# Performance work log

Hardware: AMD Instinct MI355X
Metric: run time of the kernel (lower is better)

## Reference

```python
import jax, jax.numpy as jnp
import numpy as np

N, T, D, H = 256, 128, 512, 1024


def setup_inputs() -> dict:
    key = jax.random.key(0)
    k_x, k_A, k_Wx, k_Wh, k_Wa = jax.random.split(key, 5)
    x = jax.random.normal(k_x, (N, T, D), dtype=jnp.float32)
    A = jax.random.normal(k_A, (N, H, 4, 4), dtype=jnp.float32)
    Wx = jax.random.normal(k_Wx, (D, 4 * H), dtype=jnp.float32) / np.sqrt(D)
    Wh = jax.random.normal(k_Wh, (H, 4 * H), dtype=jnp.float32) / np.sqrt(H)
    Wattn = jax.random.normal(k_Wa, (H, 4 * H), dtype=jnp.float32) / np.sqrt(H)
    b = jnp.zeros((4 * H,), dtype=jnp.float32)
    return {"x": x, "A": A, "Wx": Wx, "Wh": Wh, "Wattn": Wattn, "b": b}


def _attention_lstm(x, A, Wx, Wh, Wattn, b):
    # A: (N, H, 4, 4) -> flatten spatial to (N, H, 16)
    A_flat = A.reshape(A.shape[0], A.shape[1], -1)
    h0 = A_flat.mean(axis=2)  # (N, H)
    c0 = h0
    Hdim = h0.shape[1]
    scale = 1.0 / jnp.sqrt(jnp.asarray(Hdim, dtype=x.dtype))

    def step(carry, x_t):
        prev_h, prev_c = carry
        # scaled dot-product attention over 16 spatial locations
        scores = jnp.einsum("nh,nhs->ns", prev_h, A_flat) * scale  # (N, 16)
        w = jax.nn.softmax(scores, axis=1)
        attn = jnp.einsum("nhs,ns->nh", A_flat, w)  # (N, H)
        # fused LSTM gates
        a = x_t @ Wx + prev_h @ Wh + attn @ Wattn + b  # (N, 4H)
        i = jax.nn.sigmoid(a[:, 0:Hdim])
        f = jax.nn.sigmoid(a[:, Hdim:2 * Hdim])
        o = jax.nn.sigmoid(a[:, 2 * Hdim:3 * Hdim])
        g = jnp.tanh(a[:, 3 * Hdim:4 * Hdim])
        next_c = f * prev_c + i * g
        next_h = o * jnp.tanh(next_c)
        return (next_h, next_c), next_h

    x_tnd = jnp.swapaxes(x, 0, 1)  # (T, N, D)
    _, h_tnh = jax.lax.scan(step, (h0, c0), x_tnd)
    return jnp.swapaxes(h_tnh, 0, 1)  # (N, T, H)


def reference(x, A, Wx, Wh, Wattn, b):
    return _attention_lstm(x, A, Wx, Wh, Wattn, b)
```

## Files before the change

kernel.cpp:

```cpp
#include <hip/hip_runtime.h>
#include <math.h>

#define NB 256
#define TT 128
#define DD 512
#define HH 1024
#define KHX 1536
#define KFB 2560
#define BK 128

typedef _Float16 half_t;
typedef _Float16 half8 __attribute__((ext_vector_type(8)));
typedef _Float16 half4v __attribute__((ext_vector_type(4)));
typedef float f32x4 __attribute__((ext_vector_type(4)));


__global__ __launch_bounds__(256) void k_trans(const float* __restrict__ src,
        half_t* __restrict__ dst, int kstride, int koff, int nkt) {
    __shared__ half_t tile[64][65];
    int bk = blockIdx.x % nkt;
    int bn = blockIdx.x / nkt;
    int k0 = bk * 64, n0 = bn * 64;
    #pragma unroll
    for (int i = 0; i < 16; ++i) {
        int idx = i * 256 + threadIdx.x;
        int r = idx >> 6, c = idx & 63;
        tile[c][r] = (half_t)src[(size_t)(k0 + r) * 4096 + n0 + c];
    }
    __syncthreads();
    #pragma unroll
    for (int i = 0; i < 16; ++i) {
        int idx = i * 256 + threadIdx.x;
        int r = idx >> 6, c = idx & 63;
        dst[(size_t)(n0 + r) * kstride + koff + k0 + c] = tile[r][c];
    }
}

__global__ __launch_bounds__(256) void k_convA(const float* __restrict__ A,
        half_t* __restrict__ A16, half_t* __restrict__ AsT,
        float* __restrict__ cbuf, half_t* __restrict__ h16,
        float* __restrict__ sc0, float* __restrict__ sc1, float* __restrict__ sc2) {
    __shared__ float sred[4][16];
    int n = blockIdx.x, tid = threadIdx.x;
    float ps[16];
    #pragma unroll
    for (int s = 0; s < 16; ++s) ps[s] = 0.f;
    #pragma unroll
    for (int r = 0; r < 4; ++r) {
        int h = tid + r * 256;
        const float4* ap = (const float4*)(A + ((size_t)n * HH + h) * 16);
        float4 v0 = ap[0], v1 = ap[1], v2 = ap[2], v3 = ap[3];
        float a[16];
        a[0]=v0.x; a[1]=v0.y; a[2] =v0.z; a[3] =v0.w;
        a[4]=v1.x; a[5]=v1.y; a[6] =v1.z; a[7] =v1.w;
        a[8]=v2.x; a[9]=v2.y; a[10]=v2.z; a[11]=v2.w;
        a[12]=v3.x; a[13]=v3.y; a[14]=v3.z; a[15]=v3.w;
        float hv = 0.f;
        #pragma unroll
        for (int s = 0; s < 16; ++s) hv += a[s];
        hv *= (1.f / 16.f);
        size_t ci = (size_t)n * HH + h;
        cbuf[ci] = hv;
        h16[ci] = (half_t)hv;
        half8 q0, q1;
        #pragma unroll
        for (int s = 0; s < 8; ++s) { q0[s] = (half_t)a[s]; q1[s] = (half_t)a[s + 8]; }
        *(half8*)(A16 + ci * 16) = q0;
        *(half8*)(A16 + ci * 16 + 8) = q1;
        #pragma unroll
        for (int s = 0; s < 16; ++s)
            AsT[(size_t)n * 16 * HH + (size_t)s * HH + h] = (half_t)a[s];
        #pragma unroll
        for (int s = 0; s < 16; ++s) ps[s] += hv * a[s];
    }
    #pragma unroll
    for (int off = 32; off; off >>= 1)
        #pragma unroll
        for (int s = 0; s < 16; ++s) ps[s] += __shfl_xor(ps[s], off, 64);
    int wave = tid >> 6;
    if ((tid & 63) == 0)
        #pragma unroll
        for (int s = 0; s < 16; ++s) sred[wave][s] = ps[s];
    __syncthreads();
    if (tid < 16) {
        sc0[n * 16 + tid] = sred[0][tid] + sred[1][tid] + sred[2][tid] + sred[3][tid];
        sc1[n * 16 + tid] = 0.f;
        sc2[n * 16 + tid] = 0.f;
    }
}

__global__ __launch_bounds__(256) void k_gemm_G(const half_t* __restrict__ AsT,
        const half_t* __restrict__ WaT, half_t* __restrict__ G16) {
    __shared__ half_t sAs[16][BK + 8];
    __shared__ half_t sB[4][16][BK + 8];
    int bid = blockIdx.x;
    int n = bid >> 6, jt = bid & 63;
    int j0 = jt * 16;
    int tid = threadIdx.x, wv = tid >> 6, lane = tid & 63;
    f32x4 acc = {};
    int srB = tid >> 2, scB = (tid & 3) * 32;
    int gB = srB >> 4, jcB = srB & 15;
    for (int it = 0; it < HH / BK; ++it) {
        int k0 = it * BK;
        if (tid < 128) {
            int r = tid >> 3, c = (tid & 7) * 16;
            const uint4* sp = (const uint4*)(AsT + (size_t)n * 16 * HH + (size_t)r * HH + k0 + c);
            uint4 u0 = sp[0], u1 = sp[1];
            *(uint4*)&sAs[r][c] = u0;
            *(uint4*)&sAs[r][c + 8] = u1;
        }
        {
            const half_t* src = WaT + ((size_t)(gB * HH + j0 + jcB)) * HH + k0 + scB;
            uint4 u0 = ((const uint4*)src)[0];
            uint4 u1 = ((const uint4*)src)[1];
            uint4 u2 = ((const uint4*)src)[2];
            uint4 u3 = ((const uint4*)src)[3];
            *((uint4*)&sB[gB][jcB][scB])      = u0;
            *((uint4*)&sB[gB][jcB][scB + 8])  = u1;
            *((uint4*)&sB[gB][jcB][scB + 16]) = u2;
            *((uint4*)&sB[gB][jcB][scB + 24]) = u3;
        }
        __syncthreads();
        int row16 = lane & 15, kg = lane >> 4;
        #pragma unroll
        for (int kc = 0; kc < BK / 32; ++kc) {
            half8 bf = *(const half8*)&sB[wv][row16][kc * 32 + kg * 8];
            half8 af = *(const half8*)&sAs[row16][kc * 32 + kg * 8];
            acc = __builtin_amdgcn_mfma_f32_16x16x32_f16(af, bf, acc, 0, 0, 0);
        }
        __syncthreads();
    }
    int col = lane & 15, rbase = (lane >> 4) * 4;
    size_t jf = (size_t)wv * HH + j0 + col;
    half4v o;
    o[0] = (half_t)acc[0]; o[1] = (half_t)acc[1];
    o[2] = (half_t)acc[2]; o[3] = (half_t)acc[3];
    *(half4v*)(G16 + ((size_t)n * 4096 + jf) * 16 + rbase) = o;
}

union LdsS {
    struct {
        half_t sA[32][BK + 8];
        half_t sB[4][16][BK + 8];
    } s;
    float pe[4][32][16];
};

__global__ __launch_bounds__(256) void k_step(const float* __restrict__ x,
        const half_t* __restrict__ h16c, half_t* __restrict__ h16n,
        const half_t* __restrict__ WhxT, const half_t* __restrict__ A16,
        const half_t* __restrict__ G16, const float* __restrict__ b,
        float* __restrict__ cbuf, const float* __restrict__ scC,
        float* __restrict__ scN, float* __restrict__ scZ,
        float* __restrict__ out, int t) {
    __shared__ LdsS L;
    __shared__ float wlds[32][16];
    int bid = blockIdx.x;
    int xcd = bid & 7, slot = bid >> 3;
    int mtile = slot & 7, jtile = slot >> 3;
    int n0 = mtile * 32;
    int j0 = xcd * 128 + jtile * 16;
    int tid = threadIdx.x, wv = tid >> 6, lane = tid & 63;

    if (bid < 16) scZ[bid * 256 + tid] = 0.f;
    if (tid < 32) {
        int n = n0 + tid;
        const float4* sp = (const float4*)(scC + n * 16);
        float4 u0 = sp[0], u1 = sp[1], u2 = sp[2], u3 = sp[3];
        float sc[16] = {u0.x, u0.y, u0.z, u0.w, u1.x, u1.y, u1.z, u1.w,
                        u2.x, u2.y, u2.z, u2.w, u3.x, u3.y, u3.z, u3.w};
        float m = -1e30f;
        #pragma unroll
        for (int s = 0; s < 16; ++s) { sc[s] *= 0.03125f; m = fmaxf(m, sc[s]); }
        float den = 0.f;
        #pragma unroll
        for (int s = 0; s < 16; ++s) { sc[s] = expf(sc[s] - m); den += sc[s]; }
        float inv = 1.f / den;
        #pragma unroll
        for (int s = 0; s < 16; ++s) wlds[tid][s] = sc[s] * inv;
    }

    f32x4 acc[2] = {};
    int srA = tid >> 3, scA = (tid & 7) * 16;
    int srB = tid >> 2, scB = (tid & 3) * 32;
    int gB = srB >> 4, jcB = srB & 15;

    for (int it = 0; it < KHX / BK; ++it) {
        int k0 = it * BK;
        {
            int n = n0 + srA;
            if (k0 < DD) {
                const float* src = x + ((size_t)n * TT + t) * DD + k0 + scA;
                float4 v0 = ((const float4*)src)[0];
                float4 v1 = ((const float4*)src)[1];
                float4 v2 = ((const float4*)src)[2];
                float4 v3 = ((const float4*)src)[3];
                half8 p0, p1;
                p0[0] = (half_t)v0.x; p0[1] = (half_t)v0.y; p0[2] = (half_t)v0.z; p0[3] = (half_t)v0.w;
                p0[4] = (half_t)v1.x; p0[5] = (half_t)v1.y; p0[6] = (half_t)v1.z; p0[7] = (half_t)v1.w;
                p1[0] = (half_t)v2.x; p1[1] = (half_t)v2.y; p1[2] = (half_t)v2.z; p1[3] = (half_t)v2.w;
                p1[4] = (half_t)v3.x; p1[5] = (half_t)v3.y; p1[6] = (half_t)v3.z; p1[7] = (half_t)v3.w;
                *(half8*)&L.s.sA[srA][scA]     = p0;
                *(half8*)&L.s.sA[srA][scA + 8] = p1;
            } else {
                const half_t* srch = h16c + (size_t)n * HH + (k0 - DD) + scA;
                uint4 u0 = ((const uint4*)srch)[0];
                uint4 u1 = ((const uint4*)srch)[1];
                *((uint4*)&L.s.sA[srA][scA])     = u0;
                *((uint4*)&L.s.sA[srA][scA + 8]) = u1;
            }
        }
        {
            const half_t* src = WhxT + ((size_t)(gB * HH + j0 + jcB)) * KHX + k0 + scB;
            uint4 u0 = ((const uint4*)src)[0];
            uint4 u1 = ((const uint4*)src)[1];
            uint4 u2 = ((const uint4*)src)[2];
            uint4 u3 = ((const uint4*)src)[3];
            *((uint4*)&L.s.sB[gB][jcB][scB])      = u0;
            *((uint4*)&L.s.sB[gB][jcB][scB + 8])  = u1;
            *((uint4*)&L.s.sB[gB][jcB][scB + 16]) = u2;
            *((uint4*)&L.s.sB[gB][jcB][scB + 24]) = u3;
        }
        __syncthreads();
        int row16 = lane & 15, kg = lane >> 4;
        #pragma unroll
        for (int kc = 0; kc < BK / 32; ++kc) {
            half8 bf = *(const half8*)&L.s.sB[wv][row16][kc * 32 + kg * 8];
            #pragma unroll
            for (int m = 0; m < 2; ++m) {
                half8 af = *(const half8*)&L.s.sA[row16 + m * 16][kc * 32 + kg * 8];
                acc[m] = __builtin_amdgcn_mfma_f32_16x16x32_f16(af, bf, acc[m], 0, 0, 0);
            }
        }
        __syncthreads();
    }
    {
        int col = lane & 15, rbase = (lane >> 4) * 4;
        #pragma unroll
        for (int m = 0; m < 2; ++m)
            #pragma unroll
            for (int q = 0; q < 4; ++q)
                L.pe[wv][m * 16 + rbase + q][col] = acc[m][q];
    }
    __syncthreads();
    #pragma unroll
    for (int q2 = 0; q2 < 2; ++q2) {
        int idx = tid + q2 * 256;
        int r = idx >> 4, jc = idx & 15;
        int n = n0 + r, j = j0 + jc;
        float wv16[16];
        #pragma unroll
        for (int s = 0; s < 16; ++s) wv16[s] = wlds[r][s];
        float v[4];
        v[0] = L.pe[0][r][jc] + b[j];
        v[1] = L.pe[1][r][jc] + b[HH + j];
        v[2] = L.pe[2][r][jc] + b[2 * HH + j];
        v[3] = L.pe[3][r][jc] + b[3 * HH + j];
        #pragma unroll
        for (int g = 0; g < 4; ++g) {
            const half8* gq = (const half8*)(G16 + ((size_t)n * 4096 + g * HH + j) * 16);
            half8 ga = gq[0], gb2 = gq[1];
            float a0 = 0.f;
            #pragma unroll
            for (int s = 0; s < 8; ++s)
                a0 += wv16[s] * (float)ga[s] + wv16[s + 8] * (float)gb2[s];
            v[g] += a0;
        }
        float ig = 1.f / (1.f + expf(-v[0]));
        float fg = 1.f / (1.f + expf(-v[1]));
        float og = 1.f / (1.f + expf(-v[2]));
        float gg = tanhf(v[3]);
        size_t ci = (size_t)n * HH + j;
        float cp = cbuf[ci];
        float cn = fg * cp + ig * gg;
        cbuf[ci] = cn;
        float hv = og * tanhf(cn);
        out[((size_t)n * TT + t) * HH + j] = hv;
        h16n[ci] = (half_t)hv;
        const half8* ap = (const half8*)(A16 + ci * 16);
        half8 a0 = ap[0], a1 = ap[1];
        float p[16];
        #pragma unroll
        for (int s = 0; s < 8; ++s) { p[s] = hv * (float)a0[s]; p[s + 8] = hv * (float)a1[s]; }
        #pragma unroll
        for (int msk = 1; msk < 16; msk <<= 1)
            #pragma unroll
            for (int s = 0; s < 16; ++s) p[s] += __shfl_xor(p[s], msk, 64);
        float myp = 0.f;
        #pragma unroll
        for (int s = 0; s < 16; ++s) myp = (jc == s) ? p[s] : myp;
        atomicAdd(scN + n * 16 + jc, myp);
    }
}


__global__ __launch_bounds__(256) void fb_wconv(const float* __restrict__ Wx,
        const float* __restrict__ Wh, const float* __restrict__ Wa,
        half_t* __restrict__ WT) {
    __shared__ half_t tile[64][65];
    int bk = blockIdx.x % 40;
    int bn = blockIdx.x / 40;
    int k0 = bk * 64, n0 = bn * 64;
    #pragma unroll
    for (int i = 0; i < 16; ++i) {
        int idx = i * 256 + threadIdx.x;
        int r = idx >> 6, c = idx & 63;
        int k = k0 + r, n = n0 + c;
        float v;
        if (k < DD)            v = Wx[(size_t)k * 4096 + n];
        else if (k < DD + HH)  v = Wh[(size_t)(k - DD) * 4096 + n];
        else                   v = Wa[(size_t)(k - DD - HH) * 4096 + n];
        tile[c][r] = (half_t)v;
    }
    __syncthreads();
    #pragma unroll
    for (int i = 0; i < 16; ++i) {
        int idx = i * 256 + threadIdx.x;
        int r = idx >> 6, c = idx & 63;
        WT[(size_t)(n0 + r) * KFB + k0 + c] = tile[r][c];
    }
}

__global__ __launch_bounds__(256) void fb_init(const float* __restrict__ A,
        float* __restrict__ h0, float* __restrict__ c0) {
    int n = blockIdx.x;
    #pragma unroll
    for (int r = 0; r < 4; ++r) {
        int h = threadIdx.x + r * 256;
        const float4* ap = (const float4*)(A + ((size_t)n * HH + h) * 16);
        float s = 0.f;
        #pragma unroll
        for (int q = 0; q < 4; ++q) {
            float4 v = ap[q];
            s += v.x + v.y + v.z + v.w;
        }
        s *= (1.f / 16.f);
        h0[n * HH + h] = s;
        c0[n * HH + h] = s;
    }
}

__global__ __launch_bounds__(256) void fb_attn(const float* __restrict__ A,
        const float* __restrict__ hprev, long long hstride,
        half_t* __restrict__ h16, half_t* __restrict__ attn16) {
    __shared__ float sh[HH];
    __shared__ float sred[4][16];
    int n = blockIdx.x;
    const float* hp = hprev + (size_t)n * hstride;
    #pragma unroll
    for (int r = 0; r < 4; ++r) {
        int h = threadIdx.x + r * 256;
        float v = hp[h];
        sh[h] = v;
        h16[n * HH + h] = (half_t)v;
    }
    __syncthreads();
    float a[4][16];
    float ps[16];
    #pragma unroll
    for (int s = 0; s < 16; ++s) ps[s] = 0.f;
    #pragma unroll
    for (int r = 0; r < 4; ++r) {
        int h = threadIdx.x + r * 256;
        const float4* ap = (const float4*)(A + ((size_t)n * HH + h) * 16);
        float4 v0 = ap[0], v1 = ap[1], v2 = ap[2], v3 = ap[3];
        a[r][0] = v0.x;  a[r][1] = v0.y;  a[r][2]  = v0.z;  a[r][3]  = v0.w;
        a[r][4] = v1.x;  a[r][5] = v1.y;  a[r][6]  = v1.z;  a[r][7]  = v1.w;
        a[r][8] = v2.x;  a[r][9] = v2.y;  a[r][10] = v2.z;  a[r][11] = v2.w;
        a[r][12] = v3.x; a[r][13] = v3.y; a[r][14] = v3.z;  a[r][15] = v3.w;
        float hh = sh[h];
        #pragma unroll
        for (int s = 0; s < 16; ++s) ps[s] += hh * a[r][s];
    }
    #pragma unroll
    for (int off = 32; off; off >>= 1)
        #pragma unroll
        for (int s = 0; s < 16; ++s) ps[s] += __shfl_xor(ps[s], off, 64);
    int wave = threadIdx.x >> 6;
    if ((threadIdx.x & 63) == 0)
        #pragma unroll
        for (int s = 0; s < 16; ++s) sred[wave][s] = ps[s];
    __syncthreads();
    float sc[16], m = -1e30f;
    #pragma unroll
    for (int s = 0; s < 16; ++s) {
        sc[s] = (sred[0][s] + sred[1][s] + sred[2][s] + sred[3][s]) * 0.03125f;
        m = fmaxf(m, sc[s]);
    }
    float den = 0.f;
    #pragma unroll
    for (int s = 0; s < 16; ++s) { sc[s] = expf(sc[s] - m); den += sc[s]; }
    float inv = 1.f / den;
    #pragma unroll
    for (int r = 0; r < 4; ++r) {
        int h = threadIdx.x + r * 256;
        float acc = 0.f;
        #pragma unroll
        for (int s = 0; s < 16; ++s) acc += a[r][s] * sc[s];
        attn16[n * HH + h] = (half_t)(acc * inv);
    }
}

union LdsFB {
    struct {
        half_t sA[32][BK + 8];
        half_t sB[4][16][BK + 8];
    } s;
    float pe[4][32][16];
};

__global__ __launch_bounds__(256) void fb_gemm(const float* __restrict__ x,
        const half_t* __restrict__ h16, const half_t* __restrict__ attn16,
        const half_t* __restrict__ WT, const float* __restrict__ b,
        float* __restrict__ cbuf, float* __restrict__ out, int t) {
    __shared__ LdsFB L;
    int bid = blockIdx.x;
    int xcd = bid & 7;
    int slot = bid >> 3;
    int mtile = slot & 7;
    int jtile = slot >> 3;
    int m0 = mtile * 32;
    int j0 = xcd * 128 + jtile * 16;
    int tid = threadIdx.x;
    int wv = tid >> 6, lane = tid & 63;
    f32x4 acc[2] = {};
    int srA = tid >> 3, scA = (tid & 7) * 16;
    int srB = tid >> 2, scB = (tid & 3) * 32;
    int gB = srB >> 4, jcB = srB & 15;
    for (int it = 0; it < KFB / BK; ++it) {
        int k0 = it * BK;
        {
            int n = m0 + srA;
            if (k0 < DD) {
                const float* src = x + ((size_t)n * TT + t) * DD + k0 + scA;
                float4 v0 = ((const float4*)src)[0];
                float4 v1 = ((const float4*)src)[1];
                float4 v2 = ((const float4*)src)[2];
                float4 v3 = ((const float4*)src)[3];
                half8 p0, p1;
                p0[0] = (half_t)v0.x; p0[1] = (half_t)v0.y; p0[2] = (half_t)v0.z; p0[3] = (half_t)v0.w;
                p0[4] = (half_t)v1.x; p0[5] = (half_t)v1.y; p0[6] = (half_t)v1.z; p0[7] = (half_t)v1.w;
                p1[0] = (half_t)v2.x; p1[1] = (half_t)v2.y; p1[2] = (half_t)v2.z; p1[3] = (half_t)v2.w;
                p1[4] = (half_t)v3.x; p1[5] = (half_t)v3.y; p1[6] = (half_t)v3.z; p1[7] = (half_t)v3.w;
                *(half8*)&L.s.sA[srA][scA]     = p0;
                *(half8*)&L.s.sA[srA][scA + 8] = p1;
            } else {
                const half_t* srch = (k0 < DD + HH)
                    ? (h16    + (size_t)n * HH + (k0 - DD)      + scA)
                    : (attn16 + (size_t)n * HH + (k0 - DD - HH) + scA);
                uint4 u0 = ((const uint4*)srch)[0];
                uint4 u1 = ((const uint4*)srch)[1];
                *((uint4*)&L.s.sA[srA][scA])     = u0;
                *((uint4*)&L.s.sA[srA][scA + 8]) = u1;
            }
        }
        {
            const half_t* src = WT + ((size_t)(gB * HH + j0 + jcB)) * KFB + k0 + scB;
            uint4 u0 = ((const uint4*)src)[0];
            uint4 u1 = ((const uint4*)src)[1];
            uint4 u2 = ((const uint4*)src)[2];
            uint4 u3 = ((const uint4*)src)[3];
            *((uint4*)&L.s.sB[gB][jcB][scB])      = u0;
            *((uint4*)&L.s.sB[gB][jcB][scB + 8])  = u1;
            *((uint4*)&L.s.sB[gB][jcB][scB + 16]) = u2;
            *((uint4*)&L.s.sB[gB][jcB][scB + 24]) = u3;
        }
        __syncthreads();
        int row16 = lane & 15, kg = lane >> 4;
        #pragma unroll
        for (int kc = 0; kc < BK / 32; ++kc) {
            half8 bf = *(const half8*)&L.s.sB[wv][row16][kc * 32 + kg * 8];
            #pragma unroll
            for (int m = 0; m < 2; ++m) {
                half8 af = *(const half8*)&L.s.sA[row16 + m * 16][kc * 32 + kg * 8];
                acc[m] = __builtin_amdgcn_mfma_f32_16x16x32_f16(af, bf, acc[m], 0, 0, 0);
            }
        }
        __syncthreads();
    }
    {
        int col = lane & 15, rbase = (lane >> 4) * 4;
        #pragma unroll
        for (int m = 0; m < 2; ++m)
            #pragma unroll
            for (int q = 0; q < 4; ++q)
                L.pe[wv][m * 16 + rbase + q][col] = acc[m][q];
    }
    __syncthreads();
    #pragma unroll
    for (int q2 = 0; q2 < 2; ++q2) {
        int idx = tid + q2 * 256;
        int r = idx >> 4, jc = idx & 15;
        int n = m0 + r, j = j0 + jc;
        float vi = L.pe[0][r][jc] + b[j];
        float vf = L.pe[1][r][jc] + b[HH + j];
        float vo = L.pe[2][r][jc] + b[2 * HH + j];
        float vg = L.pe[3][r][jc] + b[3 * HH + j];
        float ig = 1.f / (1.f + expf(-vi));
        float fg = 1.f / (1.f + expf(-vf));
        float og = 1.f / (1.f + expf(-vo));
        float gg = tanhf(vg);
        size_t ci = (size_t)n * HH + j;
        float cp = cbuf[ci];
        float cn = fg * cp + ig * gg;
        cbuf[ci] = cn;
        out[((size_t)n * TT + t) * HH + j] = og * tanhf(cn);
    }
}


extern "C" void kernel_launch(void* const* d_in, const int* in_sizes, int n_in,
                              void* d_out, int out_size, void* d_ws, size_t ws_size,
                              hipStream_t stream) {
    const float* x  = (const float*)d_in[0];
    const float* A  = (const float*)d_in[1];
    const float* Wx = (const float*)d_in[2];
    const float* Wh = (const float*)d_in[3];
    const float* Wa = (const float*)d_in[4];
    const float* b  = (const float*)d_in[5];
    float* out = (float*)d_out;
    char* ws = (char*)d_ws;

    if (ws_size >= 73449472ULL) {
        half_t* WhxT = (half_t*)(ws);
        half_t* WaT  = (half_t*)(ws + 12582912);
        half_t* A16  = (half_t*)(ws + 20971520);
        half_t* AsT  = (half_t*)(ws + 29360128);
        half_t* G16  = (half_t*)(ws + 37748736);
        half_t* h16a = (half_t*)(ws + 71303168);
        half_t* h16b = (half_t*)(ws + 71827456);
        float*  cb   = (float*) (ws + 72351744);
        float*  sc0  = (float*) (ws + 73400320);
        float*  sc1  = (float*) (ws + 73416704);
        float*  sc2  = (float*) (ws + 73433088);
        float* scb[3] = {sc0, sc1, sc2};

        hipLaunchKernelGGL(k_trans, dim3(8 * 64),  dim3(256), 0, stream, Wx, WhxT, KHX, 0,   8);
        hipLaunchKernelGGL(k_trans, dim3(16 * 64), dim3(256), 0, stream, Wh, WhxT, KHX, 512, 16);
        hipLaunchKernelGGL(k_trans, dim3(16 * 64), dim3(256), 0, stream, Wa, WaT,  HH,  0,   16);
        hipLaunchKernelGGL(k_convA, dim3(256), dim3(256), 0, stream,
                           A, A16, AsT, cb, h16a, sc0, sc1, sc2);
        hipLaunchKernelGGL(k_gemm_G, dim3(NB * 64), dim3(256), 0, stream, AsT, WaT, G16);
        for (int t = 0; t < TT; ++t) {
            float* scC = scb[t % 3];
            float* scN = scb[(t + 1) % 3];
            float* scZ = scb[(t + 2) % 3];
            half_t* h16c = (t & 1) ? h16b : h16a;
            half_t* h16n = (t & 1) ? h16a : h16b;
            hipLaunchKernelGGL(k_step, dim3(512), dim3(256), 0, stream,
                               x, h16c, h16n, WhxT, A16, G16, b, cb, scC, scN, scZ, out, t);
        }
    } else {
        half_t* WT  = (half_t*)ws;
        float*  h0  = (float*)(ws + 20971520);
        float*  cb  = (float*)(ws + 22020096);
        half_t* h16 = (half_t*)(ws + 23068672);
        half_t* a16 = (half_t*)(ws + 23592960);
        hipLaunchKernelGGL(fb_wconv, dim3(2560), dim3(256), 0, stream, Wx, Wh, Wa, WT);
        hipLaunchKernelGGL(fb_init, dim3(256), dim3(256), 0, stream, A, h0, cb);
        for (int t = 0; t < TT; ++t) {
            const float* hp = (t == 0) ? h0 : (out + (size_t)(t - 1) * HH);
            long long hstride = (t == 0) ? (long long)HH : (long long)TT * HH;
            hipLaunchKernelGGL(fb_attn, dim3(256), dim3(256), 0, stream, A, hp, hstride, h16, a16);
            hipLaunchKernelGGL(fb_gemm, dim3(512), dim3(256), 0, stream,
                               x, h16, a16, WT, b, cb, out, t);
        }
    }
}
```

Measured before the change: 4.641 ms.

## Replace per-timestep kernel launches with persistent kernel using grid barrier

Adds a persistent k_steps kernel that loops over all 128 timesteps inside one launch of 512 blocks, synchronising with an atomic counter/flag grid barrier instead of launching a kernel per step. x is pre-converted to fp16, c state is kept in registers, and the gate GEMM uses a larger K tile with register prefetch. This removes per-step launch overhead and reloading of cell state, but depends on all 512 blocks being co-resident (checked via occupancy query) and adds barrier spin cost each step.

After: 4.646 ms. Within noise of the previous version (+0.1%).

```diff
diff --git a/kernel.cpp b/kernel.cpp
--- a/kernel.cpp
+++ b/kernel.cpp
@@ -8,6 +8,9 @@
 #define KHX 1536
 #define KFB 2560
 #define BK 128
+#define BKP 256
+#define NIT (KHX / BKP)
+#define NBLK 512
 
 typedef _Float16 half_t;
 typedef _Float16 half8 __attribute__((ext_vector_type(8)));
@@ -33,6 +36,20 @@
         int idx = i * 256 + threadIdx.x;
         int r = idx >> 6, c = idx & 63;
         dst[(size_t)(n0 + r) * kstride + koff + k0 + c] = tile[r][c];
+    }
+}
+
+__global__ __launch_bounds__(256) void k_convX(const float* __restrict__ x,
+        half_t* __restrict__ x16) {
+    size_t base = ((size_t)blockIdx.x * 256 + threadIdx.x) * 32;
+    #pragma unroll
+    for (int u = 0; u < 4; ++u) {
+        float4 a = ((const float4*)(x + base))[2 * u];
+        float4 c = ((const float4*)(x + base))[2 * u + 1];
+        half8 p;
+        p[0] = (half_t)a.x; p[1] = (half_t)a.y; p[2] = (half_t)a.z; p[3] = (half_t)a.w;
+        p[4] = (half_t)c.x; p[5] = (half_t)c.y; p[6] = (half_t)c.z; p[7] = (half_t)c.w;
+        ((half8*)(x16 + base))[u] = p;
     }
 }
 
@@ -137,6 +154,207 @@
     o[2] = (half_t)acc[2]; o[3] = (half_t)acc[3];
     *(half4v*)(G16 + ((size_t)n * 4096 + jf) * 16 + rbase) = o;
 }
+
+
+union LdsP {
+    struct {
+        half_t sA[32][BKP + 8];
+        half_t sB[64][BKP + 8];
+    } s;
+    float pe[4][32][16];
+};
+
+__device__ __forceinline__ void grid_sync(int* cnt, int* flag, int inst) {
+    __syncthreads();
+    if (threadIdx.x == 0) {
+        __threadfence();
+        int prev = __hip_atomic_fetch_add(cnt, 1, __ATOMIC_ACQ_REL,
+                                          __HIP_MEMORY_SCOPE_AGENT);
+        if (prev == NBLK * (inst + 1) - 1) {
+            __hip_atomic_store(flag, inst + 1, __ATOMIC_RELEASE,
+                               __HIP_MEMORY_SCOPE_AGENT);
+        } else {
+            int guard = 0;
+            while (__hip_atomic_load(flag, __ATOMIC_RELAXED,
+                                     __HIP_MEMORY_SCOPE_AGENT) < inst + 1) {
+                __builtin_amdgcn_s_sleep(2);
+                if (++guard > (1 << 24)) break;
+            }
+        }
+        __threadfence();
+    }
+    __syncthreads();
+}
+
+__global__ __launch_bounds__(256, 2) void k_steps(
+        const half_t* __restrict__ x16, const half_t* __restrict__ WhxT,
+        const half_t* __restrict__ A16, const half_t* __restrict__ G16,
+        const float* __restrict__ b, const float* __restrict__ cbuf,
+        float* __restrict__ sc0, float* __restrict__ sc1, float* __restrict__ sc2,
+        half_t* __restrict__ h16a, half_t* __restrict__ h16b,
+        float* __restrict__ out, int* __restrict__ bar) {
+    __shared__ LdsP L;
+    __shared__ float wlds[32][16];
+    int bid = blockIdx.x;
+    int xcd = bid & 7, slot = bid >> 3;
+    int mtile = slot & 7, jtile = slot >> 3;
+    int n0 = mtile * 32;
+    int j0 = xcd * 128 + jtile * 16;
+    int tid = threadIdx.x, wv = tid >> 6, lane = tid & 63;
+    int srA = tid >> 3, scA = (tid & 7) * 32;
+    int srB = tid >> 2, scB = (tid & 3) * 64;
+    int gB = srB >> 4, jcB = srB & 15;
+    int row16 = lane & 15, kg = lane >> 4;
+
+    float* scbuf[3] = {sc0, sc1, sc2};
+    int* cnt = bar;
+    int* flag = bar + 32;
+
+    float bb[2][4];
+    half8 ha[2][2];
+    float creg[2];
+    const half8* gp[2][4];
+    #pragma unroll
+    for (int q2 = 0; q2 < 2; ++q2) {
+        int idx = tid + q2 * 256;
+        int r = idx >> 4, jc = idx & 15;
+        int n = n0 + r, j = j0 + jc;
+        bb[q2][0] = b[j];          bb[q2][1] = b[HH + j];
+        bb[q2][2] = b[2 * HH + j]; bb[q2][3] = b[3 * HH + j];
+        size_t ci = (size_t)n * HH + j;
+        const half8* ap = (const half8*)(A16 + ci * 16);
+        ha[q2][0] = ap[0]; ha[q2][1] = ap[1];
+        creg[q2] = cbuf[ci];
+        #pragma unroll
+        for (int g = 0; g < 4; ++g)
+            gp[q2][g] = (const half8*)(G16 + ((size_t)n * 4096 + g * HH + j) * 16);
+    }
+    half_t* h16c = h16a;
+    half_t* h16n = h16b;
+
+    for (int t = 0; t < TT; ++t) {
+        float* scC = scbuf[t % 3];
+        float* scN = scbuf[(t + 1) % 3];
+        float* scZ = scbuf[(t + 2) % 3];
+        if (bid < 16) scZ[bid * 256 + tid] = 0.f;
+        if (tid < 32) {
+            int n = n0 + tid;
+            const float4* sp = (const float4*)(scC + n * 16);
+            float4 u0 = sp[0], u1 = sp[1], u2 = sp[2], u3 = sp[3];
+            float sc[16] = {u0.x, u0.y, u0.z, u0.w, u1.x, u1.y, u1.z, u1.w,
+                            u2.x, u2.y, u2.z, u2.w, u3.x, u3.y, u3.z, u3.w};
+            float m = -1e30f;
+            #pragma unroll
+            for (int s = 0; s < 16; ++s) { sc[s] *= 0.03125f; m = fmaxf(m, sc[s]); }
+            float den = 0.f;
+            #pragma unroll
+            for (int s = 0; s < 16; ++s) { sc[s] = expf(sc[s] - m); den += sc[s]; }
+            float inv = 1.f / den;
+            #pragma unroll
+            for (int s = 0; s < 16; ++s) wlds[tid][s] = sc[s] * inv;
+        }
+
+        f32x4 acc[2] = {};
+        uint4 rA[4], rB[8];
+        {
+            const half_t* sa = x16 + ((size_t)(n0 + srA) * TT + t) * DD + scA;
+            #pragma unroll
+            for (int u = 0; u < 4; ++u) rA[u] = ((const uint4*)sa)[u];
+            const half_t* sb = WhxT + (size_t)(gB * HH + j0 + jcB) * KHX + scB;
+            #pragma unroll
+            for (int u = 0; u < 8; ++u) rB[u] = ((const uint4*)sb)[u];
+        }
+        for (int it = 0; it < NIT; ++it) {
+            __syncthreads();
+            #pragma unroll
+            for (int u = 0; u < 4; ++u) *((uint4*)&L.s.sA[srA][scA + u * 8]) = rA[u];
+            #pragma unroll
+            for (int u = 0; u < 8; ++u)
+                *((uint4*)&L.s.sB[gB * 16 + jcB][scB + u * 8]) = rB[u];
+            __syncthreads();
+            if (it + 1 < NIT) {
+                int k0 = (it + 1) * BKP;
+                const half_t* sa = (k0 < DD)
+                    ? x16 + ((size_t)(n0 + srA) * TT + t) * DD + k0 + scA
+                    : h16c + (size_t)(n0 + srA) * HH + (k0 - DD) + scA;
+                #pragma unroll
+                for (int u = 0; u < 4; ++u) rA[u] = ((const uint4*)sa)[u];
+                const half_t* sb = WhxT + (size_t)(gB * HH + j0 + jcB) * KHX + k0 + scB;
+                #pragma unroll
+                for (int u = 0; u < 8; ++u) rB[u] = ((const uint4*)sb)[u];
+            }
+            #pragma unroll
+            for (int kc = 0; kc < BKP / 32; ++kc) {
+                half8 bf = *(const half8*)&L.s.sB[wv * 16 + row16][kc * 32 + kg * 8];
+                #pragma unroll
+                for (int m = 0; m < 2; ++m) {
+                    half8 af = *(const half8*)&L.s.sA[row16 + m * 16][kc * 32 + kg * 8];
+                    acc[m] = __builtin_amdgcn_mfma_f32_16x16x32_f16(af, bf, acc[m], 0, 0, 0);
+                }
+            }
+        }
+        __syncthreads();
+        {
+            int col = lane & 15, rbase = (lane >> 4) * 4;
+            #pragma unroll
+            for (int m = 0; m < 2; ++m)
+                #pragma unroll
+                for (int q = 0; q < 4; ++q)
+                    L.pe[wv][m * 16 + rbase + q][col] = acc[m][q];
+        }
+        __syncthreads();
+        #pragma unroll
+        for (int q2 = 0; q2 < 2; ++q2) {
+            int idx = tid + q2 * 256;
+            int r = idx >> 4, jc = idx & 15;
+            int n = n0 + r, j = j0 + jc;
+            float wv16[16];
+            #pragma unroll
+            for (int s = 0; s < 16; ++s) wv16[s] = wlds[r][s];
+            float v[4];
+            v[0] = L.pe[0][r][jc] + bb[q2][0];
+            v[1] = L.pe[1][r][jc] + bb[q2][1];
+            v[2] = L.pe[2][r][jc] + bb[q2][2];
+            v[3] = L.pe[3][r][jc] + bb[q2][3];
+            #pragma unroll
+            for (int g = 0; g < 4; ++g) {
+                half8 ga = gp[q2][g][0], gb2 = gp[q2][g][1];
+                float a0 = 0.f;
+                #pragma unroll
+                for (int s = 0; s < 8; ++s)
+                    a0 += wv16[s] * (float)ga[s] + wv16[s + 8] * (float)gb2[s];
+                v[g] += a0;
+            }
+            float ig = 1.f / (1.f + expf(-v[0]));
+            float fg = 1.f / (1.f + expf(-v[1]));
+            float og = 1.f / (1.f + expf(-v[2]));
+            float gg = tanhf(v[3]);
+            float cn = fg * creg[q2] + ig * gg;
+            creg[q2] = cn;
+            float hv = og * tanhf(cn);
+            out[((size_t)n * TT + t) * HH + j] = hv;
+            h16n[(size_t)n * HH + j] = (half_t)hv;
+            half8 a0 = ha[q2][0], a1 = ha[q2][1];
+            float p[16];
+            #pragma unroll
+            for (int s = 0; s < 8; ++s) {
+                p[s] = hv * (float)a0[s];
+                p[s + 8] = hv * (float)a1[s];
+            }
+            #pragma unroll
+            for (int msk = 1; msk < 16; msk <<= 1)
+                #pragma unroll
+                for (int s = 0; s < 16; ++s) p[s] += __shfl_xor(p[s], msk, 64);
+            float myp = 0.f;
+            #pragma unroll
+            for (int s = 0; s < 16; ++s) myp = (jc == s) ? p[s] : myp;
+            atomicAdd(scN + n * 16 + jc, myp);
+        }
+        if (t + 1 < TT) grid_sync(cnt, flag, t);
+        half_t* tmp = h16c; h16c = h16n; h16n = tmp;
+    }
+}
+
 
 union LdsS {
     struct {
@@ -521,7 +739,37 @@
     float* out = (float*)d_out;
     char* ws = (char*)d_ws;
 
-    if (ws_size >= 73449472ULL) {
+    int maxb = 0;
+    hipError_t oe = hipOccupancyMaxActiveBlocksPerMultiprocessor(&maxb, k_steps, 256, 0);
+    bool persistent_ok = (oe == hipSuccess && maxb >= 2);
+
+    if (ws_size >= 107004160ULL && persistent_ok) {
+        half_t* WhxT = (half_t*)(ws);
+        half_t* WaT  = (half_t*)(ws + 12582912);
+        half_t* A16  = (half_t*)(ws + 20971520);
+        half_t* AsT  = (half_t*)(ws + 29360128);
+        half_t* G16  = (half_t*)(ws + 37748736);
+        half_t* h16a = (half_t*)(ws + 71303168);
+        half_t* h16b = (half_t*)(ws + 71827456);
+        float*  cb   = (float*) (ws + 72351744);
+        float*  sc0  = (float*) (ws + 73400320);
+        float*  sc1  = (float*) (ws + 73416704);
+        float*  sc2  = (float*) (ws + 73433088);
+        half_t* x16  = (half_t*)(ws + 73449472);
+        int*    bar  = (int*)   (ws + 107003904);
+
+        hipLaunchKernelGGL(k_trans, dim3(8 * 64),  dim3(256), 0, stream, Wx, WhxT, KHX, 0,   8);
+        hipLaunchKernelGGL(k_trans, dim3(16 * 64), dim3(256), 0, stream, Wh, WhxT, KHX, 512, 16);
+        hipLaunchKernelGGL(k_trans, dim3(16 * 64), dim3(256), 0, stream, Wa, WaT,  HH,  0,   16);
+        hipLaunchKernelGGL(k_convX, dim3(2048), dim3(256), 0, stream, x, x16);
+        hipLaunchKernelGGL(k_convA, dim3(256), dim3(256), 0, stream,
+                           A, A16, AsT, cb, h16a, sc0, sc1, sc2);
+        hipLaunchKernelGGL(k_gemm_G, dim3(NB * 64), dim3(256), 0, stream, AsT, WaT, G16);
+        hipMemsetAsync(bar, 0, 256, stream);
+        hipLaunchKernelGGL(k_steps, dim3(NBLK), dim3(256), 0, stream,
+                           x16, WhxT, A16, G16, b, cb, sc0, sc1, sc2,
+                           h16a, h16b, out, bar);
+    } else if (ws_size >= 73449472ULL) {
         half_t* WhxT = (half_t*)(ws);
         half_t* WaT  = (half_t*)(ws + 12582912);
         half_t* A16  = (half_t*)(ws + 20971520);
```

## Replace per-timestep kernel launches with persistent kernel and grid barrier

Applied to the files above, without the earlier changes.

Adds a persistent kernel that runs all 128 LSTM timesteps inside one launch. Each block keeps its slice of the fused Wx/Wh weights resident in LDS and its G/A/bias/cell data in registers, and blocks synchronise through a global atomic barrier between steps. x is also pre-converted to fp16 so activation chunks can be double-buffered into LDS. This is meant to remove per-step launch overhead and repeated weight reloads, at the cost of relying on all 256 blocks being co-resident and on a spin barrier with a timeout guard.

Result: no change. 4.645 ms (+0.1%).

```diff
diff --git a/kernel.cpp b/kernel.cpp
--- a/kernel.cpp
+++ b/kernel.cpp
@@ -8,6 +8,8 @@
 #define KHX 1536
 #define KFB 2560
 #define BK 128
+#define NBLK2 256
+#define NCHUNK 24
 
 typedef _Float16 half_t;
 typedef _Float16 half8 __attribute__((ext_vector_type(8)));
@@ -33,6 +35,20 @@
         int idx = i * 256 + threadIdx.x;
         int r = idx >> 6, c = idx & 63;
         dst[(size_t)(n0 + r) * kstride + koff + k0 + c] = tile[r][c];
+    }
+}
+
+__global__ __launch_bounds__(256) void k_convX(const float* __restrict__ x,
+        half_t* __restrict__ x16) {
+    size_t base = ((size_t)blockIdx.x * 256 + threadIdx.x) * 32;
+    #pragma unroll
+    for (int u = 0; u < 4; ++u) {
+        float4 a = ((const float4*)(x + base))[2 * u];
+        float4 c = ((const float4*)(x + base))[2 * u + 1];
+        half8 p;
+        p[0] = (half_t)a.x; p[1] = (half_t)a.y; p[2] = (half_t)a.z; p[3] = (half_t)a.w;
+        p[4] = (half_t)c.x; p[5] = (half_t)c.y; p[6] = (half_t)c.z; p[7] = (half_t)c.w;
+        ((half8*)(x16 + base))[u] = p;
     }
 }
 
@@ -137,6 +153,254 @@
     o[2] = (half_t)acc[2]; o[3] = (half_t)acc[3];
     *(half4v*)(G16 + ((size_t)n * 4096 + jf) * 16 + rbase) = o;
 }
+
+
+struct StepLds {
+    half_t W[32][1544];
+    union {
+        half_t H[2][128][72];
+        struct {
+            float pe[128][33];
+            char  _pad[18432 - sizeof(float) * 128 * 33];
+            float ps[128][20];
+        } e;
+    } u;
+};
+
+__device__ __forceinline__ void grid_sync2(int* cnt, volatile int* flag, int inst) {
+    __syncthreads();
+    if (threadIdx.x == 0) {
+        __threadfence();
+        int prev = __hip_atomic_fetch_add(cnt, 1, __ATOMIC_ACQ_REL,
+                                          __HIP_MEMORY_SCOPE_AGENT);
+        if (prev == NBLK2 * (inst + 1) - 1) {
+            __hip_atomic_store((int*)flag, inst + 1, __ATOMIC_RELEASE,
+                               __HIP_MEMORY_SCOPE_AGENT);
+        } else {
+            int guard = 0;
+            while (__hip_atomic_load((int*)flag, __ATOMIC_RELAXED,
+                                     __HIP_MEMORY_SCOPE_AGENT) < inst + 1) {
+                __builtin_amdgcn_s_sleep(2);
+                if (++guard > (1 << 24)) break;
+            }
+        }
+        __threadfence();
+    }
+    __syncthreads();
+}
+
+__global__ __launch_bounds__(256, 1) void k_steps2(
+        const half_t* __restrict__ x16, half_t* __restrict__ h16A,
+        half_t* __restrict__ h16B, const half_t* __restrict__ WhxT,
+        const half_t* __restrict__ A16, const half_t* __restrict__ G16,
+        const float* __restrict__ b, const float* __restrict__ cbuf,
+        float* __restrict__ sc0, float* __restrict__ sc1, float* __restrict__ sc2,
+        float* __restrict__ out, int* __restrict__ bar) {
+    __shared__ StepLds L;
+    int bid = blockIdx.x;
+    int mhalf = bid & 1;
+    int jb = bid >> 1;
+    int n0 = mhalf * 128;
+    int tid = threadIdx.x, wv = tid >> 6, lane = tid & 63;
+    int la = lane & 15, kg = lane >> 4;
+    int srow = tid & 127, shalf = tid >> 7;
+    int* cnt = bar;
+    volatile int* flag = (volatile int*)(bar + 32);
+
+    {
+        int wr = tid >> 3;
+        int seg = tid & 7;
+        int g = wr >> 3, jj = wr & 7;
+        const half_t* wsrc = WhxT + (size_t)(g * HH + jb * 8 + jj) * KHX + seg * 192;
+        #pragma unroll
+        for (int i = 0; i < 24; ++i) {
+            uint4 u = ((const uint4*)wsrc)[i];
+            *(uint4*)&L.W[wr][seg * 192 + i * 8] = u;
+        }
+    }
+
+    int n_l = tid & 127;
+    int u4 = (tid >> 7) * 4;
+    int n = n0 + n_l;
+    int jbase = jb * 8 + u4;
+    half8 gq[4][8];
+    #pragma unroll
+    for (int g = 0; g < 4; ++g) {
+        const half8* gsrc = (const half8*)(G16 + ((size_t)n * 4096 + g * HH + jbase) * 16);
+        #pragma unroll
+        for (int i = 0; i < 8; ++i) gq[g][i] = gsrc[i];
+    }
+    half8 aq[8];
+    {
+        const half8* asrc = (const half8*)(A16 + ((size_t)n * HH + jbase) * 16);
+        #pragma unroll
+        for (int i = 0; i < 8; ++i) aq[i] = asrc[i];
+    }
+    float bb[4][4];
+    #pragma unroll
+    for (int g = 0; g < 4; ++g) {
+        float4 bv = *(const float4*)(b + g * HH + jbase);
+        bb[g][0] = bv.x; bb[g][1] = bv.y; bb[g][2] = bv.z; bb[g][3] = bv.w;
+    }
+    float creg[4];
+    {
+        float4 cv = *(const float4*)(cbuf + (size_t)n * HH + jbase);
+        creg[0] = cv.x; creg[1] = cv.y; creg[2] = cv.z; creg[3] = cv.w;
+    }
+
+    float* scC = sc0; float* scN = sc1; float* scZ = sc2;
+    half_t* h16c = h16A; half_t* h16n = h16B;
+
+    uint4 pA0, pA1, pA2, pA3, pB0, pB1, pB2, pB3;
+
+#define STAGE_SRC(c) ((c) < 8 \
+    ? x16 + ((size_t)(n0 + srow) * TT + t) * DD + (c) * 64 + shalf * 32 \
+    : h16c + (size_t)(n0 + srow) * HH + ((c) - 8) * 64 + shalf * 32)
+#define STAGE_LOAD_A(c) { const uint4* sp_ = (const uint4*)STAGE_SRC(c); \
+    pA0 = sp_[0]; pA1 = sp_[1]; pA2 = sp_[2]; pA3 = sp_[3]; }
+#define STAGE_LOAD_B(c) { const uint4* sp_ = (const uint4*)STAGE_SRC(c); \
+    pB0 = sp_[0]; pB1 = sp_[1]; pB2 = sp_[2]; pB3 = sp_[3]; }
+#define STAGE_WRITE_A(BUF) { \
+    *(uint4*)&L.u.H[BUF][srow][shalf * 32 + 0]  = pA0; \
+    *(uint4*)&L.u.H[BUF][srow][shalf * 32 + 8]  = pA1; \
+    *(uint4*)&L.u.H[BUF][srow][shalf * 32 + 16] = pA2; \
+    *(uint4*)&L.u.H[BUF][srow][shalf * 32 + 24] = pA3; }
+#define STAGE_WRITE_B(BUF) { \
+    *(uint4*)&L.u.H[BUF][srow][shalf * 32 + 0]  = pB0; \
+    *(uint4*)&L.u.H[BUF][srow][shalf * 32 + 8]  = pB1; \
+    *(uint4*)&L.u.H[BUF][srow][shalf * 32 + 16] = pB2; \
+    *(uint4*)&L.u.H[BUF][srow][shalf * 32 + 24] = pB3; }
+#define COMPUTE(BUF, c) { \
+    _Pragma("unroll") \
+    for (int ks = 0; ks < 2; ++ks) { \
+        half8 a0 = *(const half8*)&L.u.H[BUF][wv * 32 + la][ks * 32 + kg * 8]; \
+        half8 a1 = *(const half8*)&L.u.H[BUF][wv * 32 + 16 + la][ks * 32 + kg * 8]; \
+        half8 b0 = *(const half8*)&L.W[la][(c) * 64 + ks * 32 + kg * 8]; \
+        half8 b1 = *(const half8*)&L.W[16 + la][(c) * 64 + ks * 32 + kg * 8]; \
+        acc00 = __builtin_amdgcn_mfma_f32_16x16x32_f16(a0, b0, acc00, 0, 0, 0); \
+        acc01 = __builtin_amdgcn_mfma_f32_16x16x32_f16(a0, b1, acc01, 0, 0, 0); \
+        acc10 = __builtin_amdgcn_mfma_f32_16x16x32_f16(a1, b0, acc10, 0, 0, 0); \
+        acc11 = __builtin_amdgcn_mfma_f32_16x16x32_f16(a1, b1, acc11, 0, 0, 0); \
+    } }
+
+    for (int t = 0; t < TT; ++t) {
+        float w16[16];
+        {
+            const float4* sp = (const float4*)(scC + (size_t)n * 16);
+            float4 q0 = sp[0], q1 = sp[1], q2 = sp[2], q3 = sp[3];
+            float sc[16] = {q0.x, q0.y, q0.z, q0.w, q1.x, q1.y, q1.z, q1.w,
+                            q2.x, q2.y, q2.z, q2.w, q3.x, q3.y, q3.z, q3.w};
+            float m = -1e30f;
+            #pragma unroll
+            for (int s = 0; s < 16; ++s) { sc[s] *= 0.03125f; m = fmaxf(m, sc[s]); }
+            float den = 0.f;
+            #pragma unroll
+            for (int s = 0; s < 16; ++s) { sc[s] = expf(sc[s] - m); den += sc[s]; }
+            float inv = 1.f / den;
+            #pragma unroll
+            for (int s = 0; s < 16; ++s) w16[s] = sc[s] * inv;
+        }
+        if (bid < 16) scZ[bid * 256 + tid] = 0.f;
+
+        f32x4 acc00 = {}, acc01 = {}, acc10 = {}, acc11 = {};
+        STAGE_LOAD_A(0); STAGE_WRITE_A(0); STAGE_LOAD_B(1);
+        __syncthreads();
+        for (int d = 0; d < 12; ++d) {
+            int c0 = 2 * d, c1 = 2 * d + 1;
+            COMPUTE(0, c0);
+            STAGE_WRITE_B(1);
+            if (c0 + 2 < NCHUNK) STAGE_LOAD_A(c0 + 2);
+            __syncthreads();
+            COMPUTE(1, c1);
+            if (c0 + 2 < NCHUNK) STAGE_WRITE_A(0);
+            if (c1 + 2 < NCHUNK) STAGE_LOAD_B(c1 + 2);
+            __syncthreads();
+        }
+
+        {
+            int rbase = kg * 4;
+            #pragma unroll
+            for (int q = 0; q < 4; ++q) {
+                L.u.e.pe[wv * 32 + rbase + q][la]           = acc00[q];
+                L.u.e.pe[wv * 32 + rbase + q][16 + la]      = acc01[q];
+                L.u.e.pe[wv * 32 + 16 + rbase + q][la]      = acc10[q];
+                L.u.e.pe[wv * 32 + 16 + rbase + q][16 + la] = acc11[q];
+            }
+        }
+        __syncthreads();
+
+        float v[4][4];
+        #pragma unroll
+        for (int g = 0; g < 4; ++g)
+            #pragma unroll
+            for (int j = 0; j < 4; ++j)
+                v[g][j] = L.u.e.pe[n_l][g * 8 + u4 + j] + bb[g][j];
+        #pragma unroll
+        for (int g = 0; g < 4; ++g)
+            #pragma unroll
+            for (int j = 0; j < 4; ++j) {
+                float a0 = 0.f;
+                #pragma unroll
+                for (int s = 0; s < 16; ++s)
+                    a0 += w16[s] * (float)gq[g][j * 2 + (s >> 3)][s & 7];
+                v[g][j] += a0;
+            }
+        float hv[4];
+        #pragma unroll
+        for (int j = 0; j < 4; ++j) {
+            float ig = 1.f / (1.f + expf(-v[0][j]));
+            float fg = 1.f / (1.f + expf(-v[1][j]));
+            float og = 1.f / (1.f + expf(-v[2][j]));
+            float gg = tanhf(v[3][j]);
+            float cn = fg * creg[j] + ig * gg;
+            creg[j] = cn;
+            hv[j] = og * tanhf(cn);
+        }
+        {
+            float4 o4; o4.x = hv[0]; o4.y = hv[1]; o4.z = hv[2]; o4.w = hv[3];
+            *(float4*)(out + ((size_t)n * TT + t) * HH + jbase) = o4;
+            half4v h4; h4[0] = (half_t)hv[0]; h4[1] = (half_t)hv[1];
+            h4[2] = (half_t)hv[2]; h4[3] = (half_t)hv[3];
+            *(half4v*)(h16n + (size_t)n * HH + jbase) = h4;
+        }
+        float p[16];
+        #pragma unroll
+        for (int s = 0; s < 16; ++s) {
+            float a0 = hv[0] * (float)aq[0 * 2 + (s >> 3)][s & 7]
+                     + hv[1] * (float)aq[1 * 2 + (s >> 3)][s & 7]
+                     + hv[2] * (float)aq[2 * 2 + (s >> 3)][s & 7]
+                     + hv[3] * (float)aq[3 * 2 + (s >> 3)][s & 7];
+            p[s] = a0;
+        }
+        if (tid < 128) {
+            #pragma unroll
+            for (int s = 0; s < 16; ++s) L.u.e.ps[n_l][s] = p[s];
+        }
+        __syncthreads();
+        if (tid >= 128) {
+            #pragma unroll
+            for (int s = 0; s < 16; ++s) L.u.e.ps[n_l][s] += p[s];
+        }
+        __syncthreads();
+        {
+            int sh = (tid >> 7) * 8;
+            #pragma unroll
+            for (int i = 0; i < 8; ++i)
+                atomicAdd(scN + (size_t)n * 16 + sh + i, L.u.e.ps[n_l][sh + i]);
+        }
+
+        if (t + 1 < TT) grid_sync2(cnt, flag, t);
+        float* tmp = scC; scC = scN; scN = scZ; scZ = tmp;
+        half_t* th = h16c; h16c = h16n; h16n = th;
+    }
+#undef STAGE_SRC
+#undef STAGE_LOAD_A
+#undef STAGE_LOAD_B
+#undef STAGE_WRITE_A
+#undef STAGE_WRITE_B
+#undef COMPUTE
+}
+
 
 union LdsS {
     struct {
@@ -521,7 +785,37 @@
     float* out = (float*)d_out;
     char* ws = (char*)d_ws;
 
-    if (ws_size >= 73449472ULL) {
+    int maxb = 0;
+    hipError_t oe = hipOccupancyMaxActiveBlocksPerMultiprocessor(&maxb, k_steps2, 256, 0);
+    bool persistent_ok = (oe == hipSuccess && maxb >= 1);
+
+    if (ws_size >= 107004160ULL && persistent_ok) {
+        half_t* WhxT = (half_t*)(ws);
+        half_t* WaT  = (half_t*)(ws + 12582912);
+        half_t* A16  = (half_t*)(ws + 20971520);
+        half_t* AsT  = (half_t*)(ws + 29360128);
+        half_t* G16  = (half_t*)(ws + 37748736);
+        half_t* h16a = (half_t*)(ws + 71303168);
+        half_t* h16b = (half_t*)(ws + 71827456);
+        float*  cb   = (float*) (ws + 72351744);
+        float*  sc0  = (float*) (ws + 73400320);
+        float*  sc1  = (float*) (ws + 73416704);
+        float*  sc2  = (float*) (ws + 73433088);
+        half_t* x16  = (half_t*)(ws + 73449472);
+        int*    bar  = (int*)   (ws + 107003904);
+
+        hipLaunchKernelGGL(k_trans, dim3(8 * 64),  dim3(256), 0, stream, Wx, WhxT, KHX, 0,   8);
+        hipLaunchKernelGGL(k_trans, dim3(16 * 64), dim3(256), 0, stream, Wh, WhxT, KHX, 512, 16);
+        hipLaunchKernelGGL(k_trans, dim3(16 * 64), dim3(256), 0, stream, Wa, WaT,  HH,  0,   16);
+        hipLaunchKernelGGL(k_convX, dim3(2048), dim3(256), 0, stream, x, x16);
+        hipLaunchKernelGGL(k_convA, dim3(256), dim3(256), 0, stream,
+                           A, A16, AsT, cb, h16a, sc0, sc1, sc2);
+        hipLaunchKernelGGL(k_gemm_G, dim3(NB * 64), dim3(256), 0, stream, AsT, WaT, G16);
+        hipMemsetAsync(bar, 0, 256, stream);
+        hipLaunchKernelGGL(k_steps2, dim3(NBLK2), dim3(256), 0, stream,
+                           x16, h16a, h16b, WhxT, A16, G16, b, cb,
+                           sc0, sc1, sc2, out, bar);
+    } else if (ws_size >= 73449472ULL) {
         half_t* WhxT = (half_t*)(ws);
         half_t* WaT  = (half_t*)(ws + 12582912);
         half_t* A16  = (half_t*)(ws + 20971520);
```
